# Kernel optimization log

Hardware: AMD Instinct MI355X
Metric: run time of the kernel (lower is better)

## Reference

```python
import jax, jax.numpy as jnp
import numpy as np

H = 1024   # hidden_size
S = 1024   # seq_length
B = 32     # batch_size


def setup_inputs() -> dict:
    key = jax.random.key(0)
    k1, k2, k3, k4, k5, k6 = jax.random.split(key, 6)
    scale = 1.0 / np.sqrt(3 * H)
    return {
        "encoder_states": jax.random.normal(k1, (S, B, 2 * H), dtype=jnp.float32),
        "hidden": jax.random.normal(k2, (B, H), dtype=jnp.float32),
        "cell": jax.random.normal(k3, (B, H), dtype=jnp.float32),
        "W_attn": jax.random.normal(k4, (H, 3 * H), dtype=jnp.float32) * scale,
        "b_attn": jax.random.normal(k5, (H,), dtype=jnp.float32) * scale,
        "v_w": jax.random.normal(k6, (H,), dtype=jnp.float32) * (1.0 / np.sqrt(H)),
    }


def reference(encoder_states, hidden, cell, W_attn, b_attn, v_w):
    # cell is accepted by the original forward but unused.
    # Split the concat-linear into two projections (mathematically identical,
    # avoids materializing the repeated hidden + concat tensor):
    # cat((hidden_rep, enc), -1) @ W.T == hidden @ W[:, :H].T + enc @ W[:, H:].T
    W_h = W_attn[:, :H]          # [H, H]   multiplies decoder hidden
    W_e = W_attn[:, H:]          # [H, 2H]  multiplies encoder states
    enc = jnp.transpose(encoder_states, (1, 0, 2))          # [B, S, 2H]
    h_proj = hidden @ W_h.T + b_attn                         # [B, H], broadcast over S
    e_proj = jnp.einsum("bse,he->bsh", enc, W_e)             # [B, S, H]
    energy = jnp.tanh(h_proj[:, None, :] + e_proj)           # [B, S, H]
    attention = jnp.einsum("bsh,h->bs", energy, v_w)         # [B, S]
    return jax.nn.softmax(attention, axis=1)
```

## Files before the change

kernel.cpp:

```cpp
#include <hip/hip_runtime.h>
#include <hip/hip_bf16.h>

#define H 1024
#define S 1024
#define B 32
#define K2 2048

typedef unsigned short u16;
typedef __attribute__((ext_vector_type(8))) short short8;
typedef __attribute__((ext_vector_type(8))) unsigned short u16x8;
typedef __attribute__((ext_vector_type(4))) float floatx4;

__device__ __forceinline__ u16 f2bf(float f) {
  unsigned u = __float_as_uint(f);
  u += 0x7FFFu + ((u >> 16) & 1u);
  return (u16)(u >> 16);
}

__device__ __forceinline__ void gld_lds16(const void* g, void* l) {
  __builtin_amdgcn_global_load_lds(
      (const __attribute__((address_space(1))) unsigned int*)g,
      (__attribute__((address_space(3))) unsigned int*)l, 16, 0, 0);
}

__device__ __forceinline__ float tanh_fast(float x) {
  float t = __expf(2.0f * x);
  return 1.0f - 2.0f / (t + 1.0f);
}

__global__ void conv_we_k(const float* __restrict__ W, u16* __restrict__ dst) {
  const int h = blockIdx.x;
  const int t = threadIdx.x * 8;
  const float* sp = W + (size_t)h * 3072 + H + t;
  u16* dp = dst + (size_t)h * K2 + t;
  floatx4 x = *(const floatx4*)sp;
  floatx4 y = *(const floatx4*)(sp + 4);
  u16x8 o;
  o[0] = f2bf(x[0]); o[1] = f2bf(x[1]); o[2] = f2bf(x[2]); o[3] = f2bf(x[3]);
  o[4] = f2bf(y[0]); o[5] = f2bf(y[1]); o[6] = f2bf(y[2]); o[7] = f2bf(y[3]);
  *(u16x8*)dp = o;
}

__global__ void conv_enc_k(const float* __restrict__ enc, u16* __restrict__ dst) {
  const int sb = blockIdx.x;
  const int s = sb >> 5;
  const int b = sb & 31;
  const int t = threadIdx.x * 8;
  const float* sp = enc + (size_t)sb * K2 + t;
  u16* dp = dst + ((size_t)b * S + s) * K2 + t;
  floatx4 x = *(const floatx4*)sp;
  floatx4 y = *(const floatx4*)(sp + 4);
  u16x8 o;
  o[0] = f2bf(x[0]); o[1] = f2bf(x[1]); o[2] = f2bf(x[2]); o[3] = f2bf(x[3]);
  o[4] = f2bf(y[0]); o[5] = f2bf(y[1]); o[6] = f2bf(y[2]); o[7] = f2bf(y[3]);
  *(u16x8*)dp = o;
}

__global__ void hproj_k(const float* __restrict__ hidden, const float* __restrict__ W,
                        const float* __restrict__ b_attn, float* __restrict__ hp) {
  const int lane = threadIdx.x & 63;
  const int h = (blockIdx.x * blockDim.x + threadIdx.x) >> 6;
  float wr[16];
#pragma unroll
  for (int i = 0; i < 16; i++) wr[i] = W[(size_t)h * 3072 + lane + i * 64];
  for (int b = 0; b < B; b++) {
    float d = 0.f;
#pragma unroll
    for (int i = 0; i < 16; i++) d = fmaf(wr[i], hidden[b * H + lane + i * 64], d);
#pragma unroll
    for (int off = 32; off; off >>= 1) d += __shfl_xor(d, off);
    if (lane == 0) hp[b * H + h] = d + b_attn[h];
  }
}

#define BM 256
#define BN 256
#define BK 64
#define NKT 32

#define STG_A(BUF, MH, KT)                                                    \
  { _Pragma("unroll") for (int c_ = 0; c_ < 2; ++c_) {                        \
      const int ri_ = c_ * 64 + srow;                                         \
      const int rg_ = ((ri_ >> 6) << 7) + (MH) * 64 + (ri_ & 63);             \
      const int lg_ = sseg ^ (ri_ & 7);                                       \
      gld_lds16(Ab + (size_t)(s0 + rg_) * K2 + (KT) * BK + (lg_ << 3),        \
                (char*)&sA[BUF][MH][0] + c_ * 8192 + wv * 1024); } }

#define STG_B(BUF, NH, KT)                                                    \
  { _Pragma("unroll") for (int c_ = 0; c_ < 2; ++c_) {                        \
      const int ri_ = c_ * 64 + srow;                                         \
      const int rg_ = ((ri_ >> 5) << 6) + (NH) * 32 + (ri_ & 31);             \
      const int lg_ = sseg ^ (ri_ & 7);                                       \
      gld_lds16(Bw + (size_t)(h0 + rg_) * K2 + (KT) * BK + (lg_ << 3),        \
                (char*)&sB[BUF][NH][0] + c_ * 8192 + wv * 1024); } }

#define PHASE(BUF, MH, NH, STAGE, DRAIN)                                      \
  {                                                                           \
    short8 af_[4][2], bf_[2][2];                                              \
    _Pragma("unroll") for (int m_ = 0; m_ < 4; ++m_)                          \
      _Pragma("unroll") for (int k_ = 0; k_ < 2; ++k_)                        \
        af_[m_][k_] = *(const short8*)(&sA[BUF][MH][0] + aoff[m_][k_]);       \
    _Pragma("unroll") for (int n_ = 0; n_ < 2; ++n_)                          \
      _Pragma("unroll") for (int k_ = 0; k_ < 2; ++k_)                        \
        bf_[n_][k_] = *(const short8*)(&sB[BUF][NH][0] + boff[n_][k_]);       \
    STAGE                                                                     \
    __builtin_amdgcn_s_barrier();                                             \
    asm volatile("s_waitcnt lgkmcnt(0)" ::: "memory");                        \
    __builtin_amdgcn_sched_barrier(0);                                        \
    __builtin_amdgcn_s_setprio(1);                                            \
    _Pragma("unroll") for (int k_ = 0; k_ < 2; ++k_)                          \
      _Pragma("unroll") for (int m_ = 0; m_ < 4; ++m_)                        \
        _Pragma("unroll") for (int n_ = 0; n_ < 2; ++n_)                      \
          acc[(MH) * 4 + m_][(NH) * 2 + n_] =                                 \
              __builtin_amdgcn_mfma_f32_16x16x32_bf16(                        \
                  af_[m_][k_], bf_[n_][k_],                                   \
                  acc[(MH) * 4 + m_][(NH) * 2 + n_], 0, 0, 0);                \
    __builtin_amdgcn_s_setprio(0);                                            \
    DRAIN                                                                     \
    __builtin_amdgcn_s_barrier();                                             \
  }

__global__ __launch_bounds__(512, 2) void gemm_8ph_k(
    const u16* __restrict__ A,
    const u16* __restrict__ Bw,
    const float* __restrict__ hp, const float* __restrict__ vw,
    float* __restrict__ attn) {
  __shared__ __align__(16) u16 sA[2][2][128 * 64];
  __shared__ __align__(16) u16 sB[2][2][128 * 64];

  const int tid = threadIdx.x;
  const int lane = tid & 63;
  const int wv = tid >> 6;
  const int wr = wv >> 2;
  const int wc = wv & 3;
  const int fr = lane & 15;
  const int kgrp = lane >> 4;
  const int srow = wv * 8 + (lane >> 3);
  const int sseg = lane & 7;

  const int bid = blockIdx.x;
  const int ntile = bid >> 7;
  const int b = (bid >> 2) & 31;
  const int mtile = bid & 3;
  const int s0 = mtile * BM;
  const int h0 = ntile * BN;

  const u16* Ab = A + (size_t)b * S * K2;

  int aoff[4][2], boff[2][2];
#pragma unroll
  for (int m = 0; m < 4; ++m)
#pragma unroll
    for (int k = 0; k < 2; ++k)
      aoff[m][k] = (wr * 64 + m * 16 + fr) * 64 + ((((k << 2) + kgrp) ^ (fr & 7)) << 3);
#pragma unroll
  for (int n = 0; n < 2; ++n)
#pragma unroll
    for (int k = 0; k < 2; ++k)
      boff[n][k] = (wc * 32 + n * 16 + fr) * 64 + ((((k << 2) + kgrp) ^ (fr & 7)) << 3);

  floatx4 acc[8][4];
#pragma unroll
  for (int i = 0; i < 8; ++i)
#pragma unroll
    for (int j = 0; j < 4; ++j) acc[i][j] = (floatx4){0.f, 0.f, 0.f, 0.f};

  STG_B(0, 0, 0) STG_A(0, 0, 0) STG_A(0, 1, 0) STG_B(0, 1, 0)
  STG_B(1, 0, 1) STG_A(1, 0, 1)
  asm volatile("s_waitcnt vmcnt(4)" ::: "memory");
  __builtin_amdgcn_s_barrier();

  for (int it = 0; it < 16; ++it) {
    const int t1 = 2 * it + 1, t2 = 2 * it + 2, t3 = 2 * it + 3;
    const bool Lst = (it == 15);
    PHASE(0, 0, 0, STG_A(1, 1, t1), )
    PHASE(0, 1, 0, STG_B(1, 1, t1), )
    PHASE(0, 0, 1, if (!Lst) { STG_B(0, 0, t2) }, )
    PHASE(0, 1, 1, if (!Lst) { STG_A(0, 0, t2) },
          if (Lst) { asm volatile("s_waitcnt vmcnt(0)" ::: "memory"); }
          else     { asm volatile("s_waitcnt vmcnt(4)" ::: "memory"); } )
    PHASE(1, 0, 0, if (!Lst) { STG_A(0, 1, t2) }, )
    PHASE(1, 1, 0, if (!Lst) { STG_B(0, 1, t2) }, )
    PHASE(1, 0, 1, if (!Lst) { STG_B(1, 0, t3) }, )
    PHASE(1, 1, 1, if (!Lst) { STG_A(1, 0, t3) },
          if (!Lst) { asm volatile("s_waitcnt vmcnt(4)" ::: "memory"); } )
  }

  const int col = fr;
  const int rgrp = lane >> 4;
  float hv[4], vv[4];
#pragma unroll
  for (int nf = 0; nf < 4; ++nf) {
    const int h = h0 + wc * 64 + nf * 16 + col;
    hv[nf] = hp[b * H + h];
    vv[nf] = vw[h];
  }
#pragma unroll
  for (int mf = 0; mf < 8; ++mf) {
#pragma unroll
    for (int r = 0; r < 4; ++r) {
      float part = 0.f;
#pragma unroll
      for (int nf = 0; nf < 4; ++nf) part += tanh_fast(acc[mf][nf][r] + hv[nf]) * vv[nf];
      part += __shfl_xor(part, 1);
      part += __shfl_xor(part, 2);
      part += __shfl_xor(part, 4);
      part += __shfl_xor(part, 8);
      if (col == 0)
        atomicAdd(&attn[b * S + s0 + wr * 128 + mf * 16 + rgrp * 4 + r], part);
    }
  }
}

__global__ void softmax_k(const float* __restrict__ attn, float* __restrict__ out) {
  __shared__ float red[8];
  const int b = blockIdx.x;
  const int tid = threadIdx.x;
  const float* row = attn + b * S;
  float v[4];
#pragma unroll
  for (int i = 0; i < 4; i++) v[i] = row[tid + i * 256];
  float m = fmaxf(fmaxf(v[0], v[1]), fmaxf(v[2], v[3]));
#pragma unroll
  for (int off = 32; off; off >>= 1) m = fmaxf(m, __shfl_xor(m, off));
  if ((tid & 63) == 0) red[tid >> 6] = m;
  __syncthreads();
  m = fmaxf(fmaxf(red[0], red[1]), fmaxf(red[2], red[3]));
  float e[4], sum = 0.f;
#pragma unroll
  for (int i = 0; i < 4; i++) { e[i] = __expf(v[i] - m); sum += e[i]; }
#pragma unroll
  for (int off = 32; off; off >>= 1) sum += __shfl_xor(sum, off);
  __syncthreads();
  if ((tid & 63) == 0) red[4 + (tid >> 6)] = sum;
  __syncthreads();
  sum = red[4] + red[5] + red[6] + red[7];
  const float inv = 1.0f / sum;
#pragma unroll
  for (int i = 0; i < 4; i++) out[b * S + tid + i * 256] = e[i] * inv;
}

extern "C" void kernel_launch(void* const* d_in, const int* in_sizes, int n_in,
                              void* d_out, int out_size, void* d_ws, size_t ws_size,
                              hipStream_t stream) {
  const float* enc    = (const float*)d_in[0];
  const float* hidden = (const float*)d_in[1];
  const float* W_attn = (const float*)d_in[3];
  const float* b_attn = (const float*)d_in[4];
  const float* v_w    = (const float*)d_in[5];
  float* out = (float*)d_out;

  char* ws = (char*)d_ws;
  float* attn = (float*)ws;
  float* hp   = (float*)(ws + 131072);
  u16* Web    = (u16*)(ws + 262144);
  u16* encb   = (u16*)(ws + 4456448);

  hipMemsetAsync(attn, 0, B * S * sizeof(float), stream);
  conv_we_k<<<H, 256, 0, stream>>>(W_attn, Web);
  hproj_k<<<256, 256, 0, stream>>>(hidden, W_attn, b_attn, hp);
  conv_enc_k<<<S * B, 256, 0, stream>>>(enc, encb);
  gemm_8ph_k<<<512, 512, 0, stream>>>(encb, Web, hp, v_w, attn);
  softmax_k<<<B, 256, 0, stream>>>(attn, out);
}
```

Before: 573.8 us.

## Reuse register fragments across phases in snake order to cut LDS reads

Restructures the 8-phase GEMM mainloop to visit the (MH,NH) quadrants in snake order. A and B fragments are held in registers across phases (two B buffers), so one phase per four needs no LDS reads, and LDS read traffic drops. Global staging order and the vmcnt waits are reshuffled to keep three stages in flight. This raises register pressure at two blocks per SM and changes how the pipelined loads are timed against the buffers.

```diff
diff --git a/kernel.cpp b/kernel.cpp
--- a/kernel.cpp
+++ b/kernel.cpp
@@ -94,27 +94,34 @@
       gld_lds16(Bw + (size_t)(h0 + rg_) * K2 + (KT) * BK + (lg_ << 3),        \
                 (char*)&sB[BUF][NH][0] + c_ * 8192 + wv * 1024); } }
 
-#define PHASE(BUF, MH, NH, STAGE, DRAIN)                                      \
-  {                                                                           \
-    short8 af_[4][2], bf_[2][2];                                              \
+#define RD_A(BUF, MH)                                                         \
     _Pragma("unroll") for (int m_ = 0; m_ < 4; ++m_)                          \
       _Pragma("unroll") for (int k_ = 0; k_ < 2; ++k_)                        \
-        af_[m_][k_] = *(const short8*)(&sA[BUF][MH][0] + aoff[m_][k_]);       \
+        af[m_][k_] = *(const short8*)(&sA[BUF][MH][0] + aoff[m_][k_]);
+
+#define RD_B(DST, BUF, NH)                                                    \
     _Pragma("unroll") for (int n_ = 0; n_ < 2; ++n_)                          \
       _Pragma("unroll") for (int k_ = 0; k_ < 2; ++k_)                        \
-        bf_[n_][k_] = *(const short8*)(&sB[BUF][NH][0] + boff[n_][k_]);       \
+        DST[n_][k_] = *(const short8*)(&sB[BUF][NH][0] + boff[n_][k_]);
+
+#define MM(MH, NH, BFR)                                                       \
+    _Pragma("unroll") for (int k_ = 0; k_ < 2; ++k_)                          \
+      _Pragma("unroll") for (int m_ = 0; m_ < 4; ++m_)                        \
+        _Pragma("unroll") for (int n_ = 0; n_ < 2; ++n_)                      \
+          acc[(MH) * 4 + m_][(NH) * 2 + n_] =                                 \
+              __builtin_amdgcn_mfma_f32_16x16x32_bf16(                        \
+                  af[m_][k_], BFR[n_][k_],                                    \
+                  acc[(MH) * 4 + m_][(NH) * 2 + n_], 0, 0, 0);
+
+#define PH(READS, STAGE, MFMA_, DRAIN)                                        \
+  {                                                                           \
+    READS                                                                     \
     STAGE                                                                     \
     __builtin_amdgcn_s_barrier();                                             \
     asm volatile("s_waitcnt lgkmcnt(0)" ::: "memory");                        \
     __builtin_amdgcn_sched_barrier(0);                                        \
     __builtin_amdgcn_s_setprio(1);                                            \
-    _Pragma("unroll") for (int k_ = 0; k_ < 2; ++k_)                          \
-      _Pragma("unroll") for (int m_ = 0; m_ < 4; ++m_)                        \
-        _Pragma("unroll") for (int n_ = 0; n_ < 2; ++n_)                      \
-          acc[(MH) * 4 + m_][(NH) * 2 + n_] =                                 \
-              __builtin_amdgcn_mfma_f32_16x16x32_bf16(                        \
-                  af_[m_][k_], bf_[n_][k_],                                   \
-                  acc[(MH) * 4 + m_][(NH) * 2 + n_], 0, 0, 0);                \
+    MFMA_                                                                     \
     __builtin_amdgcn_s_setprio(0);                                            \
     DRAIN                                                                     \
     __builtin_amdgcn_s_barrier();                                             \
@@ -165,25 +172,27 @@
 #pragma unroll
     for (int j = 0; j < 4; ++j) acc[i][j] = (floatx4){0.f, 0.f, 0.f, 0.f};
 
-  STG_B(0, 0, 0) STG_A(0, 0, 0) STG_A(0, 1, 0) STG_B(0, 1, 0)
-  STG_B(1, 0, 1) STG_A(1, 0, 1)
-  asm volatile("s_waitcnt vmcnt(4)" ::: "memory");
+  short8 af[4][2], bf0[2][2], bf1[2][2];
+
+  STG_A(0, 0, 0) STG_B(0, 0, 0) STG_B(0, 1, 0) STG_A(0, 1, 0)
+  STG_A(1, 0, 1) STG_B(1, 0, 1) STG_B(1, 1, 1)
+  asm volatile("s_waitcnt vmcnt(6)" ::: "memory");
   __builtin_amdgcn_s_barrier();
 
   for (int it = 0; it < 16; ++it) {
     const int t1 = 2 * it + 1, t2 = 2 * it + 2, t3 = 2 * it + 3;
     const bool Lst = (it == 15);
-    PHASE(0, 0, 0, STG_A(1, 1, t1), )
-    PHASE(0, 1, 0, STG_B(1, 1, t1), )
-    PHASE(0, 0, 1, if (!Lst) { STG_B(0, 0, t2) }, )
-    PHASE(0, 1, 1, if (!Lst) { STG_A(0, 0, t2) },
-          if (Lst) { asm volatile("s_waitcnt vmcnt(0)" ::: "memory"); }
-          else     { asm volatile("s_waitcnt vmcnt(4)" ::: "memory"); } )
-    PHASE(1, 0, 0, if (!Lst) { STG_A(0, 1, t2) }, )
-    PHASE(1, 1, 0, if (!Lst) { STG_B(0, 1, t2) }, )
-    PHASE(1, 0, 1, if (!Lst) { STG_B(1, 0, t3) }, )
-    PHASE(1, 1, 1, if (!Lst) { STG_A(1, 0, t3) },
-          if (!Lst) { asm volatile("s_waitcnt vmcnt(4)" ::: "memory"); } )
+    PH(RD_A(0, 0) RD_B(bf0, 0, 0), STG_A(1, 1, t1), MM(0, 0, bf0), )
+    PH(RD_B(bf1, 0, 1), if (!Lst) { STG_A(0, 0, t2) }, MM(0, 1, bf1), )
+    PH(RD_A(0, 1), if (!Lst) { STG_B(0, 0, t2) }, MM(1, 1, bf1), )
+    PH(, if (!Lst) { STG_B(0, 1, t2) }, MM(1, 0, bf0),
+       if (Lst) { asm volatile("s_waitcnt vmcnt(0)" ::: "memory"); }
+       else     { asm volatile("s_waitcnt vmcnt(6)" ::: "memory"); } )
+    PH(RD_A(1, 0) RD_B(bf0, 1, 0), if (!Lst) { STG_A(0, 1, t2) }, MM(0, 0, bf0), )
+    PH(RD_B(bf1, 1, 1), if (!Lst) { STG_A(1, 0, t3) }, MM(0, 1, bf1), )
+    PH(RD_A(1, 1), if (!Lst) { STG_B(1, 0, t3) }, MM(1, 1, bf1), )
+    PH(, if (!Lst) { STG_B(1, 1, t3) }, MM(1, 0, bf0),
+       if (!Lst) { asm volatile("s_waitcnt vmcnt(6)" ::: "memory"); } )
   }
 
   const int col = fr;
```

Measured after the change: 547.0 us. -4.7%, faster.
